# Kernel optimization log

Hardware: AMD Instinct MI355X
Metric: run time of the kernel (lower is better)

Reference implementation:

```python
import jax, jax.numpy as jnp
import numpy as np

B, IN, OUT, E, H, K = 8192, 1024, 256, 16, 512, 3
EPS = 1e-10


def setup_inputs() -> dict:
    key = jax.random.key(0)
    ks = jax.random.split(key, 5)
    scaled = lambda k, shape, fan: jax.random.normal(k, shape, jnp.float32) / np.sqrt(fan)
    return {
        "x": jax.random.normal(ks[0], (B, IN), jnp.float32),
        # torch init is zeros for w_gate (degenerate ties); use small random for a meaningful reference
        "w_gate": jax.random.normal(ks[1], (IN, E), jnp.float32) * 0.02,
        "W1": scaled(ks[2], (E, IN, H), IN),
        "b1": jnp.zeros((E, H), jnp.float32),
        "W2": scaled(ks[3], (E, H, OUT), H),
        "b2": jnp.zeros((E, OUT), jnp.float32),
    }


def _cv_squared(v):
    # torch .var() is unbiased (ddof=1)
    return jnp.var(v, ddof=1) / (jnp.mean(v) ** 2 + EPS)


def reference(x, w_gate, W1, b1, W2, b2):
    # --- top-k gating (eval mode: clean logits, no noise) ---
    logits = x @ w_gate                                   # [B, E]
    top_vals, top_idx = jax.lax.top_k(logits, K)          # [B, K]
    top_gates = jax.nn.softmax(top_vals, axis=-1)         # softmax over selected k
    rows = jnp.arange(logits.shape[0])[:, None]
    gates = jnp.zeros_like(logits).at[rows, top_idx].set(top_gates)  # sparse gates [B, E]

    # --- load-balancing loss ---
    importance = gates.sum(0)
    load = (gates > 0).sum(0).astype(jnp.float32)         # _gates_to_load (eval path)
    loss = _cv_squared(importance) + _cv_squared(load)

    # --- experts (MLP stand-in; dense compute, sparse combine via zero gates) ---
    h = jax.nn.relu(jnp.einsum('bi,eih->beh', x, W1) + b1)  # [B, E, H]
    expert_out = jnp.einsum('beh,eho->beo', h, W2) + b2     # [B, E, OUT]

    # combine: equivalent to SparseDispatcher gather/split/scatter-add with gate weighting
    y = jnp.einsum('be,beo->bo', gates, expert_out)         # [B, OUT]
    return y, loss
```

## Files before the change

kernel.cpp:

```cpp
#include <hip/hip_runtime.h>

#define B_ 8192
#define IN_ 1024
#define OUT_ 256
#define E_ 16
#define KTOP 3
#define H_ 512
#define MAXSLOTS 26624
#define NTILES 208
#define HBLK 16
#define GBLK 2048

typedef __bf16 bf16;
typedef __bf16 bf16x4 __attribute__((ext_vector_type(4)));
typedef __bf16 bf16x8 __attribute__((ext_vector_type(8)));
typedef float f32x4 __attribute__((ext_vector_type(4)));

__device__ __forceinline__ void async16(const bf16* g, bf16* l) {
    __builtin_amdgcn_global_load_lds(
        (const __attribute__((address_space(1))) void*)g,
        (__attribute__((address_space(3))) void*)l,
        16, 0, 0);
}

__global__ __launch_bounds__(256) void k_stage1(
    const float* __restrict__ x, const float* __restrict__ wg,
    const float* __restrict__ W1, const float* __restrict__ W2,
    bf16* __restrict__ xbf, int* __restrict__ top_idx, float* __restrict__ top_gate,
    int* __restrict__ partial,
    bf16* __restrict__ w1t, bf16* __restrict__ w2t,
    int* __restrict__ row_ids, bf16* __restrict__ zero_row, int* __restrict__ tile_expert) {
    __shared__ __align__(16) float smem[5140];
    int bx = blockIdx.x;
    int t = threadIdx.x;
    if (bx < GBLK) {
        int* lcnt = (int*)(smem + 5124);
        int lane = t & 63;
        int row = bx * 4 + (t >> 6);
        if (t < 16) lcnt[t] = 0;
        float acc[16];
#pragma unroll
        for (int e = 0; e < 16; e++) acc[e] = 0.f;
        const float4* x4p = (const float4*)(x + (size_t)row * IN_);
        float4* swg4 = (float4*)smem;
        for (int q = 0; q < 4; q++) {
            const float4* src = (const float4*)(wg + q * 4096);
#pragma unroll
            for (int i = 0; i < 4; i++) {
                int f = i * 256 + t;
                swg4[(f >> 2) * 5 + (f & 3)] = src[f];
            }
            __syncthreads();
            float4 xv = x4p[q * 64 + lane];
            bf16x4 xb;
            xb[0] = (bf16)xv.x; xb[1] = (bf16)xv.y; xb[2] = (bf16)xv.z; xb[3] = (bf16)xv.w;
            *(bf16x4*)(xbf + (size_t)row * IN_ + (q * 64 + lane) * 4) = xb;
            float xs[4] = {xv.x, xv.y, xv.z, xv.w};
#pragma unroll
            for (int i = 0; i < 4; i++) {
                int r = lane * 4 + i;
#pragma unroll
                for (int e4 = 0; e4 < 4; e4++) {
                    float4 wv = swg4[r * 5 + e4];
                    acc[e4 * 4 + 0] += xs[i] * wv.x;
                    acc[e4 * 4 + 1] += xs[i] * wv.y;
                    acc[e4 * 4 + 2] += xs[i] * wv.z;
                    acc[e4 * 4 + 3] += xs[i] * wv.w;
                }
            }
            __syncthreads();
        }
#pragma unroll
        for (int e = 0; e < 16; e++) {
#pragma unroll
            for (int s = 32; s > 0; s >>= 1) acc[e] += __shfl_xor(acc[e], s, 64);
        }
        if (lane == 0) {
            float v[16];
#pragma unroll
            for (int e = 0; e < 16; e++) v[e] = acc[e];
            int idx[KTOP];
            float val[KTOP];
#pragma unroll
            for (int k = 0; k < KTOP; k++) {
                int best = 0;
                float bv = v[0];
                for (int e = 1; e < 16; e++) {
                    if (v[e] > bv) { bv = v[e]; best = e; }
                }
                idx[k] = best; val[k] = bv; v[best] = -1e30f;
            }
            float e1 = __expf(val[1] - val[0]);
            float e2 = __expf(val[2] - val[0]);
            float inv = 1.f / (1.f + e1 + e2);
            float g[KTOP] = {inv, e1 * inv, e2 * inv};
#pragma unroll
            for (int k = 0; k < KTOP; k++) {
                top_idx[row * KTOP + k] = idx[k];
                top_gate[row * KTOP + k] = g[k];
                atomicAdd(&lcnt[idx[k]], 1);
            }
        }
        __syncthreads();
        if (t < 16) partial[bx * 16 + t] = lcnt[t];
        return;
    }
    if (bx >= 4608) {
        if (bx < 4712) {
            row_ids[(bx - 4608) * 256 + t] = -1;
        } else {
#pragma unroll
            for (int i = 0; i < 4; i++) zero_row[t * 4 + i] = (bf16)0.f;
            if (t < NTILES) tile_expert[t] = -1;
        }
        return;
    }
    float (*tile)[65] = (float(*)[65])smem;
    const float* in; bf16* out; int Kd, Nd, e, tk, tn;
    if (bx < 4096) {
        int b1x = bx - 2048;
        in = W1; out = w1t; Kd = IN_; Nd = H_;
        e = b1x >> 7; int tt = b1x & 127; tk = tt >> 3; tn = tt & 7;
    } else {
        int b2x = bx - 4096;
        in = W2; out = w2t; Kd = H_; Nd = OUT_;
        e = b2x >> 5; int tt = b2x & 31; tk = tt >> 2; tn = tt & 3;
    }
    int r = t >> 6, c = t & 63;
    const float* src = in + ((size_t)e * Kd + tk * 64) * Nd + (size_t)tn * 64;
#pragma unroll
    for (int i = 0; i < 16; i++) {
        int rr = r + i * 4;
        tile[rr][c] = src[(size_t)rr * Nd + c];
    }
    __syncthreads();
    bf16* dst = out + ((size_t)e * Nd + tn * 64) * Kd + (size_t)tk * 64;
#pragma unroll
    for (int i = 0; i < 16; i++) {
        int rr = r + i * 4;
        dst[(size_t)rr * Kd + c] = (bf16)tile[c][rr];
    }
}

__global__ __launch_bounds__(256) void k_scatterscan(
    const int* __restrict__ top_idx, const float* __restrict__ top_gate,
    const int* __restrict__ partial,
    int* __restrict__ counts, int* __restrict__ tile_expert,
    int* __restrict__ row_ids, int* __restrict__ rowslot,
    float* __restrict__ partial_imp) {
    __shared__ int segsum[16][16];
    __shared__ int tote[16];
    __shared__ int sbase[16];
    __shared__ int lcnt[16];
    __shared__ float limp[16];
    int t = threadIdx.x;
    int blk = blockIdx.x;
    int e = t & 15, seg = t >> 4;
    int s = 0;
    for (int i = 0; i < 128; i++) s += partial[(seg * 128 + i) * 16 + e];
    segsum[seg][e] = s;
    if (t < 16) { lcnt[t] = 0; limp[t] = 0.f; }
    __syncthreads();
    if (t < 16) {
        int total = 0, pre = 0;
        for (int sg = 0; sg < 16; sg++) {
            int v = segsum[sg][t];
            total += v;
            if (sg < blk) pre += v;
        }
        tote[t] = total;
        segsum[0][t] = pre;
    }
    __syncthreads();
    if (t < 16) {
        int off = 0;
        for (int ee = 0; ee < 16; ee++) {
            if (ee == t) break;
            off += (tote[ee] + 127) & ~127;
        }
        sbase[t] = off + segsum[0][t];
        if (blk == 0) {
            counts[t] = tote[t];
            int pd = (tote[t] + 127) & ~127;
            for (int tt = off >> 7; tt < (off + pd) >> 7; ++tt) tile_expert[tt] = t;
        }
    }
    __syncthreads();
#pragma unroll
    for (int j = 0; j < 6; j++) {
        int gid = blk * 1536 + j * 256 + t;
        int ee = top_idx[gid];
        float g = top_gate[gid];
        int rank = atomicAdd(&lcnt[ee], 1);
        atomicAdd(&limp[ee], g);
        int slot = sbase[ee] + rank;
        row_ids[slot] = gid / KTOP;
        rowslot[gid] = slot;
    }
    __syncthreads();
    if (t < 16) partial_imp[blk * 16 + t] = limp[t];
}

__global__ __launch_bounds__(256) void k_gemm1(
    const bf16* __restrict__ xbf, const bf16* __restrict__ w1t,
    const float* __restrict__ b1, const int* __restrict__ row_ids,
    const int* __restrict__ tile_expert, const bf16* __restrict__ zero_row,
    bf16* __restrict__ h) {
    int e = tile_expert[blockIdx.y];
    if (e < 0) return;
    int slot_base = blockIdx.y * 128;
    int nbase = blockIdx.x * 128;
    __shared__ __align__(16) bf16 As[128 * 64];
    __shared__ __align__(16) bf16 Bs[128 * 64];
    int t = threadIdx.x;
    int rmod = (t >> 3) & 7;
    int cglob = (t & 7) ^ rmod;
    const bf16* gA[4];
    const bf16* gB[4];
#pragma unroll
    for (int j = 0; j < 4; j++) {
        int m = j * 32 + (t >> 3);
        int rid = row_ids[slot_base + m];
        gA[j] = ((rid >= 0) ? xbf + (size_t)rid * IN_ : zero_row) + cglob * 8;
        gB[j] = w1t + ((size_t)e * H_ + nbase + m) * IN_ + cglob * 8;
    }
    int w = t >> 6, lane = t & 63;
    int wm = (w >> 1) * 64, wn = (w & 1) * 64;
    int lm = lane & 15, lq = lane >> 4;
    f32x4 acc[4][4] = {};
    for (int k0 = 0; k0 < IN_; k0 += 64) {
#pragma unroll
        for (int j = 0; j < 4; j++) {
            async16(gA[j] + k0, As + (j * 256 + t) * 8);
            async16(gB[j] + k0, Bs + (j * 256 + t) * 8);
        }
        __syncthreads();
        const bf16x8* Av = (const bf16x8*)As;
        const bf16x8* Bv = (const bf16x8*)Bs;
#pragma unroll
        for (int ks = 0; ks < 2; ks++) {
            int kc = ks * 4 + lq;
            bf16x8 af[4], bfv[4];
#pragma unroll
            for (int i = 0; i < 4; i++) {
                int row = wm + i * 16 + lm;
                af[i] = Av[row * 8 + (kc ^ (row & 7))];
            }
#pragma unroll
            for (int i = 0; i < 4; i++) {
                int row = wn + i * 16 + lm;
                bfv[i] = Bv[row * 8 + (kc ^ (row & 7))];
            }
#pragma unroll
            for (int mi = 0; mi < 4; mi++)
#pragma unroll
                for (int ni = 0; ni < 4; ni++)
                    acc[mi][ni] = __builtin_amdgcn_mfma_f32_16x16x32_bf16(af[mi], bfv[ni], acc[mi][ni], 0, 0, 0);
        }
        __syncthreads();
    }
#pragma unroll
    for (int mi = 0; mi < 4; mi++) {
#pragma unroll
        for (int ni = 0; ni < 4; ni++) {
            int colg = nbase + wn + ni * 16 + lm;
            float bias = b1[e * H_ + colg];
#pragma unroll
            for (int r = 0; r < 4; r++) {
                int rowl = wm + mi * 16 + lq * 4 + r;
                float v = acc[mi][ni][r] + bias;
                v = v > 0.f ? v : 0.f;
                h[(size_t)(slot_base + rowl) * H_ + colg] = (bf16)v;
            }
        }
    }
}

__global__ __launch_bounds__(256) void k_gemm2(
    const bf16* __restrict__ h, const bf16* __restrict__ w2t,
    const float* __restrict__ b2, const int* __restrict__ tile_expert,
    bf16* __restrict__ eout) {
    int e = tile_expert[blockIdx.x];
    if (e < 0) return;
    int slot_base = blockIdx.x * 128;
    __shared__ __align__(16) bf16 As[128 * 64];
    __shared__ __align__(16) bf16 Bs[256 * 64];
    int t = threadIdx.x;
    int rmod = (t >> 3) & 7;
    int cglob = (t & 7) ^ rmod;
    const bf16* gA[4];
    const bf16* gB[8];
#pragma unroll
    for (int j = 0; j < 4; j++) {
        int m = j * 32 + (t >> 3);
        gA[j] = h + (size_t)(slot_base + m) * H_ + cglob * 8;
    }
#pragma unroll
    for (int j = 0; j < 8; j++) {
        int m = j * 32 + (t >> 3);
        gB[j] = w2t + ((size_t)e * OUT_ + m) * H_ + cglob * 8;
    }
    int w = t >> 6, lane = t & 63;
    int wm = (w >> 1) * 64, wn = (w & 1) * 128;
    int lm = lane & 15, lq = lane >> 4;
    f32x4 acc[4][8] = {};
    for (int k0 = 0; k0 < H_; k0 += 64) {
#pragma unroll
        for (int j = 0; j < 4; j++) async16(gA[j] + k0, As + (j * 256 + t) * 8);
#pragma unroll
        for (int j = 0; j < 8; j++) async16(gB[j] + k0, Bs + (j * 256 + t) * 8);
        __syncthreads();
        const bf16x8* Av = (const bf16x8*)As;
        const bf16x8* Bv = (const bf16x8*)Bs;
#pragma unroll
        for (int ks = 0; ks < 2; ks++) {
            int kc = ks * 4 + lq;
            bf16x8 af[4], bfv[8];
#pragma unroll
            for (int i = 0; i < 4; i++) {
                int row = wm + i * 16 + lm;
                af[i] = Av[row * 8 + (kc ^ (row & 7))];
            }
#pragma unroll
            for (int i = 0; i < 8; i++) {
                int row = wn + i * 16 + lm;
                bfv[i] = Bv[row * 8 + (kc ^ (row & 7))];
            }
#pragma unroll
            for (int mi = 0; mi < 4; mi++)
#pragma unroll
                for (int ni = 0; ni < 8; ni++)
                    acc[mi][ni] = __builtin_amdgcn_mfma_f32_16x16x32_bf16(af[mi], bfv[ni], acc[mi][ni], 0, 0, 0);
        }
        __syncthreads();
    }
#pragma unroll
    for (int mi = 0; mi < 4; mi++) {
#pragma unroll
        for (int ni = 0; ni < 8; ni++) {
            int colg = wn + ni * 16 + lm;
            float bias = b2[e * OUT_ + colg];
#pragma unroll
            for (int r = 0; r < 4; r++) {
                int rowl = wm + mi * 16 + lq * 4 + r;
                eout[(size_t)(slot_base + rowl) * OUT_ + colg] = (bf16)(acc[mi][ni][r] + bias);
            }
        }
    }
}

__global__ __launch_bounds__(256) void k_combine(
    const bf16* __restrict__ eout, const int* __restrict__ rowslot,
    const float* __restrict__ top_gate, float* __restrict__ y,
    const float* __restrict__ partial_imp, const int* __restrict__ counts,
    float* __restrict__ loss_out) {
    int t = threadIdx.x;
    if (blockIdx.x == B_ / 4) {
        __shared__ float imp[16];
        if (t < 16) {
            float s = 0.f;
#pragma unroll
            for (int b = 0; b < HBLK; b++) s += partial_imp[b * 16 + t];
            imp[t] = s;
        }
        __syncthreads();
        if (t == 0) {
            float si = 0.f, sl = 0.f;
            for (int e = 0; e < E_; e++) { si += imp[e]; sl += (float)counts[e]; }
            float mi_ = si / (float)E_, ml_ = sl / (float)E_;
            float vi = 0.f, vl = 0.f;
            for (int e = 0; e < E_; e++) {
                float d = imp[e] - mi_; vi += d * d;
                float d2 = (float)counts[e] - ml_; vl += d2 * d2;
            }
            vi /= (float)(E_ - 1); vl /= (float)(E_ - 1);
            *loss_out = vi / (mi_ * mi_ + 1e-10f) + vl / (ml_ * ml_ + 1e-10f);
        }
        return;
    }
    int b = blockIdx.x * 4 + (t >> 6);
    int lane = t & 63;
    int s0 = rowslot[b * 3], s1 = rowslot[b * 3 + 1], s2 = rowslot[b * 3 + 2];
    float g0 = top_gate[b * 3], g1 = top_gate[b * 3 + 1], g2 = top_gate[b * 3 + 2];
    bf16x4 v0 = *(const bf16x4*)(eout + (size_t)s0 * OUT_ + lane * 4);
    bf16x4 v1 = *(const bf16x4*)(eout + (size_t)s1 * OUT_ + lane * 4);
    bf16x4 v2 = *(const bf16x4*)(eout + (size_t)s2 * OUT_ + lane * 4);
    float4 r;
    r.x = g0 * (float)v0[0] + g1 * (float)v1[0] + g2 * (float)v2[0];
    r.y = g0 * (float)v0[1] + g1 * (float)v1[1] + g2 * (float)v2[1];
    r.z = g0 * (float)v0[2] + g1 * (float)v1[2] + g2 * (float)v2[2];
    r.w = g0 * (float)v0[3] + g1 * (float)v1[3] + g2 * (float)v2[3];
    ((float4*)y)[(size_t)b * 64 + lane] = r;
}

extern "C" void kernel_launch(void* const* d_in, const int* in_sizes, int n_in,
                              void* d_out, int out_size, void* d_ws, size_t ws_size,
                              hipStream_t stream) {
    (void)in_sizes; (void)n_in; (void)out_size; (void)ws_size;
    const float* x = (const float*)d_in[0];
    const float* wgate = (const float*)d_in[1];
    const float* W1 = (const float*)d_in[2];
    const float* b1 = (const float*)d_in[3];
    const float* W2 = (const float*)d_in[4];
    const float* b2 = (const float*)d_in[5];
    float* y = (float*)d_out;

    char* p = (char*)d_ws;
    auto alloc = [&](size_t bytes) {
        char* q = p;
        p += (bytes + 255) & ~(size_t)255;
        return q;
    };
    bf16* xbf = (bf16*)alloc((size_t)B_ * IN_ * 2);
    bf16* w1t = (bf16*)alloc((size_t)E_ * H_ * IN_ * 2);
    bf16* w2t = (bf16*)alloc((size_t)E_ * OUT_ * H_ * 2);
    bf16* h = (bf16*)alloc((size_t)MAXSLOTS * H_ * 2);
    int* row_ids = (int*)alloc((size_t)MAXSLOTS * 4);
    int* rowslot = (int*)alloc((size_t)B_ * KTOP * 4);
    int* top_idx = (int*)alloc((size_t)B_ * KTOP * 4);
    float* top_gate = (float*)alloc((size_t)B_ * KTOP * 4);
    int* counts = (int*)alloc(E_ * 4);
    int* partial = (int*)alloc((size_t)GBLK * E_ * 4);
    float* partial_imp = (float*)alloc(HBLK * E_ * 4);
    int* tile_expert = (int*)alloc(NTILES * 4);
    bf16* zero_row = (bf16*)alloc(IN_ * 2);
    bf16* eout = (bf16*)xbf;

    k_stage1<<<dim3(4713), dim3(256), 0, stream>>>(
        x, wgate, W1, W2, xbf, top_idx, top_gate, partial, w1t, w2t,
        row_ids, zero_row, tile_expert);
    k_scatterscan<<<dim3(HBLK), dim3(256), 0, stream>>>(
        top_idx, top_gate, partial, counts, tile_expert, row_ids, rowslot, partial_imp);
    k_gemm1<<<dim3(H_ / 128, NTILES), dim3(256), 0, stream>>>(
        xbf, w1t, b1, row_ids, tile_expert, zero_row, h);
    k_gemm2<<<dim3(NTILES), dim3(256), 0, stream>>>(
        h, w2t, b2, tile_expert, eout);
    k_combine<<<dim3(B_ / 4 + 1), dim3(256), 0, stream>>>(
        eout, rowslot, top_gate, y, partial_imp, counts, y + (size_t)B_ * OUT_);
}
```

Before: 208.4 us.

## Fuse expert GEMM1 and GEMM2 into one kernel keeping hidden tile in LDS

Merges the two expert MLP GEMMs into a single kernel where each 128-row tile computes the hidden activations in two 256-wide chunks, stores them swizzled in shared memory, and immediately multiplies by W2. This removes the global write and reread of the hidden tensor and one kernel launch. In exchange the grid shrinks to 208 blocks of 512 threads with large LDS use, which reduces parallelism and leaves some CUs idle.

```diff
diff --git a/kernel.cpp b/kernel.cpp
--- a/kernel.cpp
+++ b/kernel.cpp
@@ -201,149 +201,136 @@
     if (t < 16) partial_imp[blk * 16 + t] = limp[t];
 }
 
-__global__ __launch_bounds__(256) void k_gemm1(
+__global__ __launch_bounds__(512) void k_fused(
     const bf16* __restrict__ xbf, const bf16* __restrict__ w1t,
-    const float* __restrict__ b1, const int* __restrict__ row_ids,
+    const float* __restrict__ b1, const bf16* __restrict__ w2t,
+    const float* __restrict__ b2, const int* __restrict__ row_ids,
     const int* __restrict__ tile_expert, const bf16* __restrict__ zero_row,
-    bf16* __restrict__ h) {
-    int e = tile_expert[blockIdx.y];
-    if (e < 0) return;
-    int slot_base = blockIdx.y * 128;
-    int nbase = blockIdx.x * 128;
-    __shared__ __align__(16) bf16 As[128 * 64];
-    __shared__ __align__(16) bf16 Bs[128 * 64];
-    int t = threadIdx.x;
-    int rmod = (t >> 3) & 7;
-    int cglob = (t & 7) ^ rmod;
-    const bf16* gA[4];
-    const bf16* gB[4];
-#pragma unroll
-    for (int j = 0; j < 4; j++) {
-        int m = j * 32 + (t >> 3);
-        int rid = row_ids[slot_base + m];
-        gA[j] = ((rid >= 0) ? xbf + (size_t)rid * IN_ : zero_row) + cglob * 8;
-        gB[j] = w1t + ((size_t)e * H_ + nbase + m) * IN_ + cglob * 8;
-    }
-    int w = t >> 6, lane = t & 63;
-    int wm = (w >> 1) * 64, wn = (w & 1) * 64;
-    int lm = lane & 15, lq = lane >> 4;
-    f32x4 acc[4][4] = {};
-    for (int k0 = 0; k0 < IN_; k0 += 64) {
-#pragma unroll
-        for (int j = 0; j < 4; j++) {
-            async16(gA[j] + k0, As + (j * 256 + t) * 8);
-            async16(gB[j] + k0, Bs + (j * 256 + t) * 8);
-        }
-        __syncthreads();
-        const bf16x8* Av = (const bf16x8*)As;
-        const bf16x8* Bv = (const bf16x8*)Bs;
-#pragma unroll
-        for (int ks = 0; ks < 2; ks++) {
-            int kc = ks * 4 + lq;
-            bf16x8 af[4], bfv[4];
-#pragma unroll
-            for (int i = 0; i < 4; i++) {
-                int row = wm + i * 16 + lm;
-                af[i] = Av[row * 8 + (kc ^ (row & 7))];
-            }
-#pragma unroll
-            for (int i = 0; i < 4; i++) {
-                int row = wn + i * 16 + lm;
-                bfv[i] = Bv[row * 8 + (kc ^ (row & 7))];
-            }
-#pragma unroll
-            for (int mi = 0; mi < 4; mi++)
-#pragma unroll
-                for (int ni = 0; ni < 4; ni++)
-                    acc[mi][ni] = __builtin_amdgcn_mfma_f32_16x16x32_bf16(af[mi], bfv[ni], acc[mi][ni], 0, 0, 0);
-        }
-        __syncthreads();
-    }
-#pragma unroll
-    for (int mi = 0; mi < 4; mi++) {
-#pragma unroll
-        for (int ni = 0; ni < 4; ni++) {
-            int colg = nbase + wn + ni * 16 + lm;
-            float bias = b1[e * H_ + colg];
-#pragma unroll
-            for (int r = 0; r < 4; r++) {
-                int rowl = wm + mi * 16 + lq * 4 + r;
-                float v = acc[mi][ni][r] + bias;
-                v = v > 0.f ? v : 0.f;
-                h[(size_t)(slot_base + rowl) * H_ + colg] = (bf16)v;
-            }
-        }
-    }
-}
-
-__global__ __launch_bounds__(256) void k_gemm2(
-    const bf16* __restrict__ h, const bf16* __restrict__ w2t,
-    const float* __restrict__ b2, const int* __restrict__ tile_expert,
     bf16* __restrict__ eout) {
     int e = tile_expert[blockIdx.x];
     if (e < 0) return;
     int slot_base = blockIdx.x * 128;
-    __shared__ __align__(16) bf16 As[128 * 64];
-    __shared__ __align__(16) bf16 Bs[256 * 64];
+    __shared__ __align__(16) bf16 smem[57344];
+    bf16* hs  = smem;
+    bf16* As  = smem + 32768;
+    bf16* Bs1 = smem + 40960;
+    bf16* Bs2 = smem + 32768;
     int t = threadIdx.x;
     int rmod = (t >> 3) & 7;
     int cglob = (t & 7) ^ rmod;
-    const bf16* gA[4];
-    const bf16* gB[8];
+    const bf16* gA[2];
+#pragma unroll
+    for (int j = 0; j < 2; j++) {
+        int m = j * 64 + (t >> 3);
+        int rid = row_ids[slot_base + m];
+        gA[j] = ((rid >= 0) ? xbf + (size_t)rid * IN_ : zero_row) + cglob * 8;
+    }
+    const bf16* gB1[4];
 #pragma unroll
     for (int j = 0; j < 4; j++) {
-        int m = j * 32 + (t >> 3);
-        gA[j] = h + (size_t)(slot_base + m) * H_ + cglob * 8;
-    }
-#pragma unroll
-    for (int j = 0; j < 8; j++) {
-        int m = j * 32 + (t >> 3);
-        gB[j] = w2t + ((size_t)e * OUT_ + m) * H_ + cglob * 8;
+        int m = j * 64 + (t >> 3);
+        gB1[j] = w1t + ((size_t)e * H_ + m) * IN_ + cglob * 8;
+    }
+    const bf16* gB2[4];
+#pragma unroll
+    for (int j = 0; j < 4; j++) {
+        int m = j * 64 + (t >> 3);
+        gB2[j] = w2t + ((size_t)e * OUT_ + m) * H_ + cglob * 8;
     }
     int w = t >> 6, lane = t & 63;
-    int wm = (w >> 1) * 64, wn = (w & 1) * 128;
+    int wm = (w & 1) * 64, wn = (w >> 1) * 64;
     int lm = lane & 15, lq = lane >> 4;
-    f32x4 acc[4][8] = {};
-    for (int k0 = 0; k0 < H_; k0 += 64) {
-#pragma unroll
-        for (int j = 0; j < 4; j++) async16(gA[j] + k0, As + (j * 256 + t) * 8);
-#pragma unroll
-        for (int j = 0; j < 8; j++) async16(gB[j] + k0, Bs + (j * 256 + t) * 8);
+    f32x4 acc2[4][4] = {};
+    for (int c = 0; c < 2; c++) {
+        f32x4 acc1[4][4] = {};
+        for (int k0 = 0; k0 < IN_; k0 += 64) {
+#pragma unroll
+            for (int j = 0; j < 2; j++) async16(gA[j] + k0, As + (j * 512 + t) * 8);
+#pragma unroll
+            for (int j = 0; j < 4; j++)
+                async16(gB1[j] + (size_t)c * (256 * IN_) + k0, Bs1 + (j * 512 + t) * 8);
+            __syncthreads();
+            const bf16x8* Av = (const bf16x8*)As;
+            const bf16x8* Bv = (const bf16x8*)Bs1;
+#pragma unroll
+            for (int ks = 0; ks < 2; ks++) {
+                int kc = ks * 4 + lq;
+                bf16x8 af[4], bfv[4];
+#pragma unroll
+                for (int i = 0; i < 4; i++) {
+                    int row = wm + i * 16 + lm;
+                    af[i] = Av[row * 8 + (kc ^ (row & 7))];
+                }
+#pragma unroll
+                for (int i = 0; i < 4; i++) {
+                    int row = wn + i * 16 + lm;
+                    bfv[i] = Bv[row * 8 + (kc ^ (row & 7))];
+                }
+#pragma unroll
+                for (int mi = 0; mi < 4; mi++)
+#pragma unroll
+                    for (int ni = 0; ni < 4; ni++)
+                        acc1[mi][ni] = __builtin_amdgcn_mfma_f32_16x16x32_bf16(af[mi], bfv[ni], acc1[mi][ni], 0, 0, 0);
+            }
+            __syncthreads();
+        }
+        const float* b1c = b1 + e * H_ + c * 256;
+#pragma unroll
+        for (int mi = 0; mi < 4; mi++) {
+#pragma unroll
+            for (int ni = 0; ni < 4; ni++) {
+                int col = wn + ni * 16 + lm;
+                float bias = b1c[col];
+#pragma unroll
+                for (int r = 0; r < 4; r++) {
+                    int row = wm + mi * 16 + lq * 4 + r;
+                    float v = acc1[mi][ni][r] + bias;
+                    v = v > 0.f ? v : 0.f;
+                    hs[row * 256 + (((col >> 3) ^ (row & 7)) << 3) + (col & 7)] = (bf16)v;
+                }
+            }
+        }
         __syncthreads();
-        const bf16x8* Av = (const bf16x8*)As;
-        const bf16x8* Bv = (const bf16x8*)Bs;
-#pragma unroll
-        for (int ks = 0; ks < 2; ks++) {
-            int kc = ks * 4 + lq;
-            bf16x8 af[4], bfv[8];
-#pragma unroll
-            for (int i = 0; i < 4; i++) {
-                int row = wm + i * 16 + lm;
-                af[i] = Av[row * 8 + (kc ^ (row & 7))];
-            }
-#pragma unroll
-            for (int i = 0; i < 8; i++) {
-                int row = wn + i * 16 + lm;
-                bfv[i] = Bv[row * 8 + (kc ^ (row & 7))];
-            }
-#pragma unroll
-            for (int mi = 0; mi < 4; mi++)
-#pragma unroll
-                for (int ni = 0; ni < 8; ni++)
-                    acc[mi][ni] = __builtin_amdgcn_mfma_f32_16x16x32_bf16(af[mi], bfv[ni], acc[mi][ni], 0, 0, 0);
-        }
-        __syncthreads();
+        for (int s = 0; s < 4; s++) {
+#pragma unroll
+            for (int j = 0; j < 4; j++)
+                async16(gB2[j] + c * 256 + s * 64, Bs2 + (j * 512 + t) * 8);
+            __syncthreads();
+            const bf16x8* Hv = (const bf16x8*)hs;
+            const bf16x8* B2v = (const bf16x8*)Bs2;
+#pragma unroll
+            for (int ks = 0; ks < 2; ks++) {
+                int kc = ks * 4 + lq;
+                bf16x8 af[4], bfv[4];
+#pragma unroll
+                for (int i = 0; i < 4; i++) {
+                    int row = wm + i * 16 + lm;
+                    af[i] = Hv[row * 32 + ((s * 8 + kc) ^ (row & 7))];
+                }
+#pragma unroll
+                for (int i = 0; i < 4; i++) {
+                    int row = wn + i * 16 + lm;
+                    bfv[i] = B2v[row * 8 + (kc ^ (row & 7))];
+                }
+#pragma unroll
+                for (int mi = 0; mi < 4; mi++)
+#pragma unroll
+                    for (int ni = 0; ni < 4; ni++)
+                        acc2[mi][ni] = __builtin_amdgcn_mfma_f32_16x16x32_bf16(af[mi], bfv[ni], acc2[mi][ni], 0, 0, 0);
+            }
+            __syncthreads();
+        }
     }
 #pragma unroll
     for (int mi = 0; mi < 4; mi++) {
 #pragma unroll
-        for (int ni = 0; ni < 8; ni++) {
+        for (int ni = 0; ni < 4; ni++) {
             int colg = wn + ni * 16 + lm;
             float bias = b2[e * OUT_ + colg];
 #pragma unroll
             for (int r = 0; r < 4; r++) {
                 int rowl = wm + mi * 16 + lq * 4 + r;
-                eout[(size_t)(slot_base + rowl) * OUT_ + colg] = (bf16)(acc[mi][ni][r] + bias);
+                eout[(size_t)(slot_base + rowl) * OUT_ + colg] = (bf16)(acc2[mi][ni][r] + bias);
             }
         }
     }
@@ -414,7 +401,7 @@
     bf16* xbf = (bf16*)alloc((size_t)B_ * IN_ * 2);
     bf16* w1t = (bf16*)alloc((size_t)E_ * H_ * IN_ * 2);
     bf16* w2t = (bf16*)alloc((size_t)E_ * OUT_ * H_ * 2);
-    bf16* h = (bf16*)alloc((size_t)MAXSLOTS * H_ * 2);
+    bf16* eout = (bf16*)alloc((size_t)MAXSLOTS * OUT_ * 2);
     int* row_ids = (int*)alloc((size_t)MAXSLOTS * 4);
     int* rowslot = (int*)alloc((size_t)B_ * KTOP * 4);
     int* top_idx = (int*)alloc((size_t)B_ * KTOP * 4);
@@ -424,17 +411,14 @@
     float* partial_imp = (float*)alloc(HBLK * E_ * 4);
     int* tile_expert = (int*)alloc(NTILES * 4);
     bf16* zero_row = (bf16*)alloc(IN_ * 2);
-    bf16* eout = (bf16*)xbf;
 
     k_stage1<<<dim3(4713), dim3(256), 0, stream>>>(
         x, wgate, W1, W2, xbf, top_idx, top_gate, partial, w1t, w2t,
         row_ids, zero_row, tile_expert);
     k_scatterscan<<<dim3(HBLK), dim3(256), 0, stream>>>(
         top_idx, top_gate, partial, counts, tile_expert, row_ids, rowslot, partial_imp);
-    k_gemm1<<<dim3(H_ / 128, NTILES), dim3(256), 0, stream>>>(
-        xbf, w1t, b1, row_ids, tile_expert, zero_row, h);
-    k_gemm2<<<dim3(NTILES), dim3(256), 0, stream>>>(
-        h, w2t, b2, tile_expert, eout);
+    k_fused<<<dim3(NTILES), dim3(512), 0, stream>>>(
+        xbf, w1t, b1, w2t, b2, row_ids, tile_expert, zero_row, eout);
     k_combine<<<dim3(B_ / 4 + 1), dim3(256), 0, stream>>>(
         eout, rowslot, top_gate, y, partial_imp, counts, y + (size_t)B_ * OUT_);
 }
```

Measured after the change: 217.1 us. 4.2% more time.
